# Optimization experiments

Hardware: AMD Instinct MI355X
Metric: run time of the kernel (lower is better)

Reference implementation:

```python
import jax, jax.numpy as jnp
import numpy as np

N_NODES = 50000
N_EDGES = 640000
D_IN = 128
D_H = 128


def gcn_conv(x, edge_index_sl, W, b, n_nodes):
    # x: [N, d_in]; edge_index_sl: [2, E+N] (self-loops already appended)
    h = x @ W  # [N, d_out]
    row, col = edge_index_sl[0], edge_index_sl[1]
    deg = jax.ops.segment_sum(jnp.ones(row.shape[0], dtype=x.dtype), col,
                              num_segments=n_nodes)
    dis = jnp.where(deg > 0, jax.lax.rsqrt(jnp.maximum(deg, 1e-12)), 0.0)
    norm = dis[row] * dis[col]  # [E+N]
    msg = h[row] * norm[:, None]  # gather + scale, [E+N, d_out]
    out = jax.ops.segment_sum(msg, col, num_segments=n_nodes)  # scatter-add
    return out + b


def setup_inputs() -> dict:
    key = jax.random.key(0)
    ks = jax.random.split(key, 9)
    x = jax.random.normal(ks[0], (N_NODES, D_IN), dtype=jnp.float32)
    edge_index = jax.random.randint(ks[1], (2, N_EDGES), 0, N_NODES, dtype=jnp.int64)
    s0 = 1.0 / np.sqrt(D_IN)
    s1 = 1.0 / np.sqrt(D_H)
    W0 = jax.random.uniform(ks[2], (D_IN, D_H), jnp.float32, -s0, s0)
    b0 = jnp.zeros((D_H,), jnp.float32)
    W1 = jax.random.uniform(ks[3], (D_H, D_H), jnp.float32, -s1, s1)
    b1 = jnp.zeros((D_H,), jnp.float32)
    W2 = jax.random.uniform(ks[4], (D_H, D_H), jnp.float32, -s1, s1)
    b2 = jnp.zeros((D_H,), jnp.float32)
    return {"x": x, "edge_index": edge_index, "W0": W0, "b0": b0,
            "W1": W1, "b1": b1, "W2": W2, "b2": b2}


def reference(x, edge_index, W0, b0, W1, b1, W2, b2):
    n = x.shape[0]
    # GCNConv adds self-loops: append (i, i) for every node.
    loops = jnp.arange(n, dtype=edge_index.dtype)
    ei = jnp.concatenate([edge_index, jnp.stack([loops, loops])], axis=1)
    h = x
    for W, b in ((W0, b0), (W1, b1), (W2, b2)):
        h = gcn_conv(h, ei, W, b, n)
        h = jax.nn.relu(h)  # dropout is identity in eval mode
    return h
```

## Files before the change

kernel.cpp:

```cpp
#include <hip/hip_runtime.h>
#include <hip/hip_bf16.h>

#define D 128
#define CAP 64
typedef _Float16 f16;
typedef unsigned short u16;
typedef f16 f16x8 __attribute__((ext_vector_type(8)));
typedef f16 f16x2 __attribute__((ext_vector_type(2)));
typedef float f32x4 __attribute__((ext_vector_type(4)));



__global__ void scatter_cvt_kernel(const int* __restrict__ row, const int* __restrict__ col,
                                   int* __restrict__ fill, u16* __restrict__ ssrc, int E,
                                   const float* __restrict__ W0, const float* __restrict__ W1,
                                   const float* __restrict__ W2,
                                   const float* __restrict__ b0, const float* __restrict__ b1,
                                   const float* __restrict__ b2,
                                   f16* __restrict__ WT, float* __restrict__ bperm) {
    const int EB = (E + 255) >> 8;
    const int b = blockIdx.x;
    if (b < EB) {
        int i = b * 256 + threadIdx.x;
        if (i < E) {
            int d = col[i];
            int p = atomicAdd(&fill[d], 1);
            if (p < CAP) ssrc[(size_t)d * CAP + p] = (u16)row[i];
        }
    } else {
        int id = (b - EB) * 256 + threadIdx.x;
        if (id < 49152) {
            int l = id >> 14;
            int e = id & 16383;
            int j = e >> 7;
            int nn = e & 127;
            int k = (l == 0) ? j : ((j >> 3) + 16 * (j & 7));
            const float* W = (l == 0) ? W0 : (l == 1) ? W1 : W2;
            WT[(size_t)l * 16384 + nn * 128 + j] = (f16)W[k * 128 + nn];
        } else if (id < 49536) {
            int j = id - 49152;
            int l = j >> 7;
            int pos = j & 127;
            int c = 16 * (pos & 7) + (pos >> 3);
            const float* bb = (l == 0) ? b0 : (l == 1) ? b1 : b2;
            bperm[l * 128 + pos] = bb[c];
        }
    }
}


template <bool A_F32>
__global__ __launch_bounds__(256) void gemm_mfma(const void* __restrict__ Aptr,
                                                 const f16* __restrict__ WT,
                                                 const int* __restrict__ fill,
                                                 f16* __restrict__ H, int n) {
    __shared__ f16 sW[128 * 128];
    const int tid  = threadIdx.x;
    const int w    = tid >> 6, lane = tid & 63;
    const int q    = lane >> 4, c = lane & 15;
    const int row0 = blockIdx.x * 64;

    int arow = row0 + w * 16 + c;
    if (arow >= n) arow = n - 1;

    f16x8 afr[4];
    if (A_F32) {
        float4 x0[4], x1[4];
        #pragma unroll
        for (int t = 0; t < 4; ++t) {
            const float* src = (const float*)Aptr + (size_t)arow * D + (t * 4 + q) * 8;
            x0[t] = *(const float4*)src;
            x1[t] = *(const float4*)(src + 4);
        }
        #pragma unroll
        for (int t = 0; t < 4; ++t) {
            f16x8 h;
            h[0] = (f16)x0[t].x; h[1] = (f16)x0[t].y; h[2] = (f16)x0[t].z; h[3] = (f16)x0[t].w;
            h[4] = (f16)x1[t].x; h[5] = (f16)x1[t].y; h[6] = (f16)x1[t].z; h[7] = (f16)x1[t].w;
            afr[t] = h;
        }
    } else {
        #pragma unroll
        for (int t = 0; t < 4; ++t)
            afr[t] = *(const f16x8*)((const f16*)Aptr + (size_t)arow * D + (t * 4 + q) * 8);
    }

    #pragma unroll
    for (int i = 0; i < 8; ++i) {
        int f = i * 256 + tid;
        int r = f >> 4, b = f & 15;
        int u = (r << 4) | (b ^ (r & 15));
        *(f16x8*)&sW[u * 8] = *(const f16x8*)&WT[(size_t)r * D + b * 8];
    }
    __syncthreads();

    f32x4 acc[8];
    #pragma unroll
    for (int nt = 0; nt < 8; ++nt) acc[nt] = (f32x4)0.f;

    #pragma unroll
    for (int nt = 0; nt < 8; ++nt) {
        const int rn = nt * 16 + c;
        #pragma unroll
        for (int t = 0; t < 4; ++t) {
            f16x8 bfr = *(const f16x8*)&sW[(((rn << 4) | ((t * 4 + q) ^ c))) * 8];
            acc[nt] = __builtin_amdgcn_mfma_f32_16x16x32_f16(afr[t], bfr, acc[nt], 0, 0, 0);
        }
    }

    const int rbase = row0 + w * 16 + q * 4;
    int4 fv4 = *(const int4*)&fill[rbase];
    #pragma unroll
    for (int reg = 0; reg < 4; ++reg) {
        int grow = rbase + reg;
        if (grow < n) {
            int fv = (reg == 0) ? fv4.x : (reg == 1) ? fv4.y : (reg == 2) ? fv4.z : fv4.w;
            float dv = rsqrtf((float)(fv + 1));
            f16x8 hh;
            #pragma unroll
            for (int nt = 0; nt < 8; ++nt) hh[nt] = (f16)(acc[nt][reg] * dv);
            *(f16x8*)&H[(size_t)grow * D + c * 8] = hh;
        }
    }
}


template <bool LAST>
__global__ __launch_bounds__(256) void agg_kernel(const f16* __restrict__ H,
                                                  const int* __restrict__ fill,
                                                  const u16* __restrict__ ssrc,
                                                  const float* __restrict__ bperm,
                                                  float* __restrict__ out,
                                                  f16* __restrict__ act, int n) {
    const int v    = (blockIdx.x * 256 + threadIdx.x) >> 6;
    const int lane = threadIdx.x & 63;
    if (v >= n) return;
    const int fo = lane * 2;

    f16x2 hv = *(const f16x2*)&H[(size_t)v * D + fo];
    float ax = (float)hv[0], ay = (float)hv[1];

    const int truedeg = fill[v];
    int deg = truedeg > CAP ? CAP : truedeg;
    int e = v * CAP;
    const int e1 = e + deg;
    for (; e + 8 <= e1; e += 8) {
        int s0 = ssrc[e],     s1 = ssrc[e + 1], s2 = ssrc[e + 2], s3 = ssrc[e + 3];
        int s4 = ssrc[e + 4], s5 = ssrc[e + 5], s6 = ssrc[e + 6], s7 = ssrc[e + 7];
        f16x2 h0 = *(const f16x2*)&H[(size_t)s0 * D + fo];
        f16x2 h1 = *(const f16x2*)&H[(size_t)s1 * D + fo];
        f16x2 h2 = *(const f16x2*)&H[(size_t)s2 * D + fo];
        f16x2 h3 = *(const f16x2*)&H[(size_t)s3 * D + fo];
        f16x2 h4 = *(const f16x2*)&H[(size_t)s4 * D + fo];
        f16x2 h5 = *(const f16x2*)&H[(size_t)s5 * D + fo];
        f16x2 h6 = *(const f16x2*)&H[(size_t)s6 * D + fo];
        f16x2 h7 = *(const f16x2*)&H[(size_t)s7 * D + fo];
        float px = ((float)h0[0] + (float)h1[0]) + ((float)h2[0] + (float)h3[0]);
        float py = ((float)h0[1] + (float)h1[1]) + ((float)h2[1] + (float)h3[1]);
        float qx = ((float)h4[0] + (float)h5[0]) + ((float)h6[0] + (float)h7[0]);
        float qy = ((float)h4[1] + (float)h5[1]) + ((float)h6[1] + (float)h7[1]);
        ax += px + qx;
        ay += py + qy;
    }
    for (; e + 2 <= e1; e += 2) {
        int s0 = ssrc[e], s1 = ssrc[e + 1];
        f16x2 h0 = *(const f16x2*)&H[(size_t)s0 * D + fo];
        f16x2 h1 = *(const f16x2*)&H[(size_t)s1 * D + fo];
        ax += (float)h0[0] + (float)h1[0];
        ay += (float)h0[1] + (float)h1[1];
    }
    if (e < e1) {
        int s = ssrc[e];
        f16x2 h = *(const f16x2*)&H[(size_t)s * D + fo];
        ax += (float)h[0];
        ay += (float)h[1];
    }

    const float dv = rsqrtf((float)(truedeg + 1));
    float2 bb = *(const float2*)&bperm[fo];
    float rx = fmaxf(fmaf(dv, ax, bb.x), 0.f);
    float ry = fmaxf(fmaf(dv, ay, bb.y), 0.f);
    if (LAST) {
        const int col0 = 16 * ((2 * lane) & 7) + (lane >> 2);
        out[(size_t)v * D + col0]      = rx;
        out[(size_t)v * D + col0 + 16] = ry;
    } else {
        f16x2 res;
        res[0] = (f16)rx; res[1] = (f16)ry;
        *(f16x2*)&act[(size_t)v * D + fo] = res;
    }
}


extern "C" void kernel_launch(void* const* d_in, const int* in_sizes, int n_in,
                              void* d_out, int out_size, void* d_ws, size_t ws_size,
                              hipStream_t stream) {
    const float* x  = (const float*)d_in[0];
    const int*   ei = (const int*)d_in[1];
    const float* W0 = (const float*)d_in[2];
    const float* b0 = (const float*)d_in[3];
    const float* W1 = (const float*)d_in[4];
    const float* b1 = (const float*)d_in[5];
    const float* W2 = (const float*)d_in[6];
    const float* b2 = (const float*)d_in[7];
    float* out = (float*)d_out;

    const int n = in_sizes[0] / D;
    const int E = in_sizes[1] / 2;
    const int n_pad = (n + 63) & ~63;
    const int* row = ei;
    const int* col = ei + E;
    const int EB = (E + 255) / 256;

    char* w = (char*)d_ws;
    size_t o = 0;
    f16* hbuf = (f16*)(w + o); o += (size_t)n_pad * D * 2;
    f16* act  = (f16*)(w + o); o += (size_t)n_pad * D * 2;
    f16* WT   = (f16*)(w + o); o += (size_t)3 * 16384 * 2;
    o = (o + 63) & ~(size_t)63;
    float* bperm = (float*)(w + o); o += 3 * 128 * 4;
    int* fill = (int*)(w + o); o += (size_t)n_pad * 4;
    o = (o + 127) & ~(size_t)127;
    u16* ssrc = (u16*)(w + o);

    hipMemsetAsync(fill, 0, (size_t)n_pad * 4, stream);
    scatter_cvt_kernel<<<EB + 194, 256, 0, stream>>>(row, col, fill, ssrc, E,
                                                     W0, W1, W2, b0, b1, b2, WT, bperm);

    const int gblocks = (n + 63) / 64;
    const int ablocks = (n + 3) / 4;

    gemm_mfma<true><<<gblocks, 256, 0, stream>>>(x, WT, fill, hbuf, n);
    agg_kernel<false><<<ablocks, 256, 0, stream>>>(hbuf, fill, ssrc, bperm, out, act, n);
    gemm_mfma<false><<<gblocks, 256, 0, stream>>>(act, WT + 16384, fill, hbuf, n);
    agg_kernel<false><<<ablocks, 256, 0, stream>>>(hbuf, fill, ssrc, bperm + 128, out, act, n);
    gemm_mfma<false><<<gblocks, 256, 0, stream>>>(act, WT + 2 * 16384, fill, hbuf, n);
    agg_kernel<true><<<ablocks, 256, 0, stream>>>(hbuf, fill, ssrc, bperm + 256, out, act, n);
}
```

Measured before the change: 244.1 us.

## Process two nodes per wavefront with branchless padded gathers in aggregation

The aggregation kernel now assigns each half-wavefront (32 lanes) to one node, with each lane handling 4 features via f16x4 loads instead of 2. Neighbor indices are loaded 16 at a time as vectors and prefetched one block ahead. Out-of-range slots are redirected to a zeroed padding row that the GEMM now writes, so the gather loop is fixed-length and free of branches. This raises memory-level parallelism and load width, at the cost of wasted gathers for low-degree nodes and for the shorter of the two nodes in each wavefront.

```diff
diff --git a/kernel.cpp b/kernel.cpp
--- a/kernel.cpp
+++ b/kernel.cpp
@@ -6,7 +6,7 @@
 typedef _Float16 f16;
 typedef unsigned short u16;
 typedef f16 f16x8 __attribute__((ext_vector_type(8)));
-typedef f16 f16x2 __attribute__((ext_vector_type(2)));
+typedef f16 f16x4 __attribute__((ext_vector_type(4)));
 typedef float f32x4 __attribute__((ext_vector_type(4)));
 
 
@@ -120,6 +120,9 @@
             #pragma unroll
             for (int nt = 0; nt < 8; ++nt) hh[nt] = (f16)(acc[nt][reg] * dv);
             *(f16x8*)&H[(size_t)grow * D + c * 8] = hh;
+        } else {
+            const f16x8 z = {};
+            *(f16x8*)&H[(size_t)grow * D + c * 8] = z;
         }
     }
 }
@@ -132,62 +135,74 @@
                                                   const float* __restrict__ bperm,
                                                   float* __restrict__ out,
                                                   f16* __restrict__ act, int n) {
-    const int v    = (blockIdx.x * 256 + threadIdx.x) >> 6;
-    const int lane = threadIdx.x & 63;
-    if (v >= n) return;
-    const int fo = lane * 2;
-
-    f16x2 hv = *(const f16x2*)&H[(size_t)v * D + fo];
-    float ax = (float)hv[0], ay = (float)hv[1];
-
+    const int tid  = threadIdx.x;
+    const int wid  = (blockIdx.x << 2) | (tid >> 6);
+    const int half = (tid >> 5) & 1;
+    const int l    = tid & 31;
+    int v = wid * 2 + half;
+    const bool valid = (v < n);
+    if (!valid) v = n - 1;
+    const int fo = l * 4;
+    const int zr = n;
+
+    const u16* sp = &ssrc[(size_t)v * CAP];
+
+    int4 sv0 = *(const int4*)sp;
+    int4 sv1 = *(const int4*)(sp + 8);
+    f16x4 hv = *(const f16x4*)&H[(size_t)v * D + fo];
     const int truedeg = fill[v];
+
     int deg = truedeg > CAP ? CAP : truedeg;
-    int e = v * CAP;
-    const int e1 = e + deg;
-    for (; e + 8 <= e1; e += 8) {
-        int s0 = ssrc[e],     s1 = ssrc[e + 1], s2 = ssrc[e + 2], s3 = ssrc[e + 3];
-        int s4 = ssrc[e + 4], s5 = ssrc[e + 5], s6 = ssrc[e + 6], s7 = ssrc[e + 7];
-        f16x2 h0 = *(const f16x2*)&H[(size_t)s0 * D + fo];
-        f16x2 h1 = *(const f16x2*)&H[(size_t)s1 * D + fo];
-        f16x2 h2 = *(const f16x2*)&H[(size_t)s2 * D + fo];
-        f16x2 h3 = *(const f16x2*)&H[(size_t)s3 * D + fo];
-        f16x2 h4 = *(const f16x2*)&H[(size_t)s4 * D + fo];
-        f16x2 h5 = *(const f16x2*)&H[(size_t)s5 * D + fo];
-        f16x2 h6 = *(const f16x2*)&H[(size_t)s6 * D + fo];
-        f16x2 h7 = *(const f16x2*)&H[(size_t)s7 * D + fo];
-        float px = ((float)h0[0] + (float)h1[0]) + ((float)h2[0] + (float)h3[0]);
-        float py = ((float)h0[1] + (float)h1[1]) + ((float)h2[1] + (float)h3[1]);
-        float qx = ((float)h4[0] + (float)h5[0]) + ((float)h6[0] + (float)h7[0]);
-        float qy = ((float)h4[1] + (float)h5[1]) + ((float)h6[1] + (float)h7[1]);
-        ax += px + qx;
-        ay += py + qy;
-    }
-    for (; e + 2 <= e1; e += 2) {
-        int s0 = ssrc[e], s1 = ssrc[e + 1];
-        f16x2 h0 = *(const f16x2*)&H[(size_t)s0 * D + fo];
-        f16x2 h1 = *(const f16x2*)&H[(size_t)s1 * D + fo];
-        ax += (float)h0[0] + (float)h1[0];
-        ay += (float)h0[1] + (float)h1[1];
-    }
-    if (e < e1) {
-        int s = ssrc[e];
-        f16x2 h = *(const f16x2*)&H[(size_t)s * D + fo];
-        ax += (float)h[0];
-        ay += (float)h[1];
+    int nb  = (deg + 15) >> 4;
+    int nbo = __shfl_xor(nb, 32);
+    const int nbmax = nb > nbo ? nb : nbo;
+
+    float a0 = (float)hv[0], a1 = (float)hv[1], a2 = (float)hv[2], a3 = (float)hv[3];
+
+    for (int b = 0; b < nbmax; ++b) {
+        const int4 c0 = sv0, c1 = sv1;
+        if (b + 1 < nbmax) {
+            sv0 = *(const int4*)(sp + (b + 1) * 16);
+            sv1 = *(const int4*)(sp + (b + 1) * 16 + 8);
+        }
+        const int rem = deg - b * 16;
+        const int wv[8] = {c0.x, c0.y, c0.z, c0.w, c1.x, c1.y, c1.z, c1.w};
+        f16x4 g[16];
+        #pragma unroll
+        for (int j = 0; j < 16; ++j) {
+            int iv = (wv[j >> 1] >> ((j & 1) * 16)) & 0xffff;
+            iv = (j < rem) ? iv : zr;
+            g[j] = *(const f16x4*)&H[(size_t)iv * D + fo];
+        }
+        #pragma unroll
+        for (int j = 0; j < 16; j += 4) {
+            a0 += ((float)g[j][0] + (float)g[j + 1][0]) + ((float)g[j + 2][0] + (float)g[j + 3][0]);
+            a1 += ((float)g[j][1] + (float)g[j + 1][1]) + ((float)g[j + 2][1] + (float)g[j + 3][1]);
+            a2 += ((float)g[j][2] + (float)g[j + 1][2]) + ((float)g[j + 2][2] + (float)g[j + 3][2]);
+            a3 += ((float)g[j][3] + (float)g[j + 1][3]) + ((float)g[j + 2][3] + (float)g[j + 3][3]);
+        }
     }
 
     const float dv = rsqrtf((float)(truedeg + 1));
-    float2 bb = *(const float2*)&bperm[fo];
-    float rx = fmaxf(fmaf(dv, ax, bb.x), 0.f);
-    float ry = fmaxf(fmaf(dv, ay, bb.y), 0.f);
-    if (LAST) {
-        const int col0 = 16 * ((2 * lane) & 7) + (lane >> 2);
-        out[(size_t)v * D + col0]      = rx;
-        out[(size_t)v * D + col0 + 16] = ry;
-    } else {
-        f16x2 res;
-        res[0] = (f16)rx; res[1] = (f16)ry;
-        *(f16x2*)&act[(size_t)v * D + fo] = res;
+    const float4 bb = *(const float4*)&bperm[fo];
+    float r0 = fmaxf(fmaf(dv, a0, bb.x), 0.f);
+    float r1 = fmaxf(fmaf(dv, a1, bb.y), 0.f);
+    float r2 = fmaxf(fmaf(dv, a2, bb.z), 0.f);
+    float r3 = fmaxf(fmaf(dv, a3, bb.w), 0.f);
+
+    if (valid) {
+        if (LAST) {
+            const int cb = (l & 1) * 64 + (l >> 1);
+            float* op = out + (size_t)v * D + cb;
+            op[0]  = r0;
+            op[16] = r1;
+            op[32] = r2;
+            op[48] = r3;
+        } else {
+            f16x4 res;
+            res[0] = (f16)r0; res[1] = (f16)r1; res[2] = (f16)r2; res[3] = (f16)r3;
+            *(f16x4*)&act[(size_t)v * D + fo] = res;
+        }
     }
 }
 
@@ -207,7 +222,7 @@
 
     const int n = in_sizes[0] / D;
     const int E = in_sizes[1] / 2;
-    const int n_pad = (n + 63) & ~63;
+    const int n_pad = (n + 64) & ~63;
     const int* row = ei;
     const int* col = ei + E;
     const int EB = (E + 255) / 256;
@@ -227,8 +242,9 @@
     scatter_cvt_kernel<<<EB + 194, 256, 0, stream>>>(row, col, fill, ssrc, E,
                                                      W0, W1, W2, b0, b1, b2, WT, bperm);
 
-    const int gblocks = (n + 63) / 64;
-    const int ablocks = (n + 3) / 4;
+    const int gblocks = n_pad >> 6;
+    const int aggwaves = (n + 1) >> 1;
+    const int ablocks = (aggwaves + 3) >> 2;
 
     gemm_mfma<true><<<gblocks, 256, 0, stream>>>(x, WT, fill, hbuf, n);
     agg_kernel<false><<<ablocks, 256, 0, stream>>>(hbuf, fill, ssrc, bperm, out, act, n);
```

Result: faster. 235.3 us (-3.6%).
